# Kernel optimization log

Measured on AMD Instinct MI355X. Metric: run time of the kernel, lower is better.

## Reference

```python
import jax, jax.numpy as jnp
import numpy as np

N, E, C, H, EDGE_DIM, HID = 50000, 800000, 128, 8, 64, 512
D = C // H  # head dim = out_channels_conv


def layer_norm(x, g, b, eps=1e-5):
    mu = x.mean(-1, keepdims=True)
    var = ((x - mu) ** 2).mean(-1, keepdims=True)
    return (x - mu) * jax.lax.rsqrt(var + eps) * g + b


def _lin_init(k, fan_in, fan_out):
    s = 1.0 / np.sqrt(fan_in)
    kw, kb = jax.random.split(k)
    w = jax.random.uniform(kw, (fan_in, fan_out), minval=-s, maxval=s, dtype=jnp.float32)
    b = jax.random.uniform(kb, (fan_out,), minval=-s, maxval=s, dtype=jnp.float32)
    return w, b


def setup_inputs() -> dict:
    key = jax.random.key(0)
    ks = jax.random.split(key, 16)
    wq, bq = _lin_init(ks[0], C, C)
    wk, bk = _lin_init(ks[1], C, C)
    wv, bv = _lin_init(ks[2], C, C)
    ws, bs = _lin_init(ks[3], C, C)          # lin_self
    we, be = _lin_init(ks[4], EDGE_DIM, C)   # lin_edge
    wp, bp = _lin_init(ks[5], C, C)          # projection
    w1, b1 = _lin_init(ks[6], C, HID)        # node_dst_mlp[0]
    w2, b2 = _lin_init(ks[7], HID, C)        # node_dst_mlp[2]
    x = jax.random.normal(ks[8], (N, C), dtype=jnp.float32)
    edge_attr = jax.random.normal(ks[9], (E, EDGE_DIM), dtype=jnp.float32)
    edge_index = jax.random.randint(ks[10], (2, E), 0, N, dtype=jnp.int64)
    return dict(
        x=x, edge_attr=edge_attr, edge_index=edge_index,
        wq=wq, bq=bq, wk=wk, bk=bk, wv=wv, bv=bv, ws=ws, bs=bs,
        we=we, be=be, wp=wp, bp=bp, w1=w1, b1=b1, w2=w2, b2=b2,
        ln1_g=jnp.ones((C,), jnp.float32), ln1_b=jnp.zeros((C,), jnp.float32),
        ln2_g=jnp.ones((C,), jnp.float32), ln2_b=jnp.zeros((C,), jnp.float32),
    )


def reference(x, edge_attr, edge_index,
              wq, bq, wk, bk, wv, bv, ws, bs, we, be, wp, bp,
              w1, b1, w2, b2, ln1_g, ln1_b, ln2_g, ln2_b):
    src, dst = edge_index[0], edge_index[1]

    x_skip = x
    xn = layer_norm(x, ln1_g, ln1_b)                       # layer_norm_attention
    x_r = xn @ ws + bs                                     # lin_self residual
    q = (xn @ wq + bq).reshape(N, H, D)
    k = (xn @ wk + bk).reshape(N, H, D)
    v = (xn @ wv + bv).reshape(N, H, D)
    e = (edge_attr @ we + be).reshape(E, H, D)             # lin_edge (edge_pre_mlp = Identity)

    # edge-indexed multi-head attention: softmax over incoming edges per dst node
    ke = k[src] + e                                        # [E,H,D]
    alpha = jnp.einsum('ehd,ehd->eh', q[dst], ke) / np.sqrt(D)   # [E,H]
    amax = jax.lax.stop_gradient(jax.ops.segment_max(alpha, dst, num_segments=N))
    ex = jnp.exp(alpha - amax[dst])
    den = jax.ops.segment_sum(ex, dst, num_segments=N)
    w = ex / (den[dst] + 1e-16)                            # [E,H]
    out = jax.ops.segment_sum(w[:, :, None] * (v[src] + e), dst, num_segments=N)  # [N,H,D]
    out = out.reshape(N, C)

    out = (out + x_r) @ wp + bp                            # projection
    out = out + x_skip
    h = layer_norm(out, ln2_g, ln2_b)                      # layer_norm_mlp_dst
    h = jax.nn.gelu(h @ w1 + b1) @ w2 + b2                 # node_dst_mlp
    nodes_new = out + h
    return nodes_new, edge_attr
```

## Files before the change

kernel.cpp:

```cpp
#include <hip/hip_runtime.h>
#include <hip/hip_bf16.h>
#include <cstdio>

#define NN 50000
#define NE 800000
#define CC 128
#define EDIM 64
#define HIDN 512

using bf16 = __hip_bfloat16;
typedef short sh8 __attribute__((ext_vector_type(8)));
typedef float f32x4 __attribute__((ext_vector_type(4)));

static __device__ __forceinline__ float b2f(bf16 v){ return __bfloat162float(v); }
static __device__ __forceinline__ bf16 f2b(float v){ return __float2bfloat16(v); }
static __device__ __forceinline__ float u2f(unsigned short u){
    union { unsigned int i; float f; } w; w.i = ((unsigned int)u) << 16; return w.f;
}
static __device__ __forceinline__ unsigned short f2u(float f){
    bf16 b = __float2bfloat16(f);
    return *reinterpret_cast<unsigned short*>(&b);
}
static __device__ __forceinline__ float2 loadbf2(const bf16* p){
    __hip_bfloat162 v = *reinterpret_cast<const __hip_bfloat162*>(p);
    return make_float2(__bfloat162float(v.x), __bfloat162float(v.y));
}
static __device__ __forceinline__ float gelu_tanh(float x){
    const float c = 0.7978845608028654f;
    float u = c * (x + 0.044715f * x * x * x);
    return x / (1.0f + __expf(-2.0f * u));
}

constexpr size_t AL(size_t x){ return (x + 255) & ~(size_t)255; }
constexpr size_t OFF_FLAG = 0;
constexpr size_t OFF_DEG  = 256;
constexpr size_t OFF_ROW  = AL(OFF_DEG + (size_t)(NN + 1) * 4);
constexpr size_t OFF_CUR  = AL(OFF_ROW + (size_t)(NN + 1) * 4);
constexpr size_t OFF_EPOS = AL(OFF_CUR + (size_t)NN * 4);
constexpr size_t OFF_SRC  = AL(OFF_EPOS + (size_t)NE * 4);
constexpr size_t OFF_DST  = AL(OFF_SRC + (size_t)NE * 4);
constexpr size_t OFF_QC   = AL(OFF_DST + (size_t)NE * 4);
constexpr size_t OFF_KC   = AL(OFF_QC  + (size_t)NN * CC * 2);
constexpr size_t OFF_VC   = AL(OFF_KC  + (size_t)NN * CC * 2);
constexpr size_t OFF_ATT  = AL(OFF_VC  + (size_t)NN * CC * 2);
constexpr size_t OFF_PRM  = AL(OFF_ATT + (size_t)NN * CC * 2);
constexpr size_t PRM_ELEMS = 4*(16384+128) + 8192+128 + 16384+128 + 65536+512 + 65536+128 + 4*128;
constexpr size_t OFF_ALP  = AL(OFF_PRM + PRM_ELEMS * 2);
constexpr size_t OFF_VP   = AL(OFF_ALP + (size_t)NE * 8 * 4);
constexpr size_t OFF_XRC  = AL(OFF_VP + (size_t)NE * CC * 2);
constexpr size_t OFF_WFQ  = AL(OFF_XRC + (size_t)NN * CC * 2);
constexpr size_t OFF_WFK  = OFF_WFQ + 32768;
constexpr size_t OFF_WFV  = OFF_WFK + 32768;
constexpr size_t OFF_WFS  = OFF_WFV + 32768;
constexpr size_t OFF_WFP  = OFF_WFS + 32768;
constexpr size_t OFF_WF1  = OFF_WFP + 32768;
constexpr size_t OFF_WF2  = OFF_WF1 + 131072;
constexpr size_t OFF_WFE  = OFF_WF2 + 131072;
constexpr size_t OFF_BSUM = OFF_WFE + 16384;
constexpr size_t WS_NEED  = OFF_BSUM + 256;

__global__ void k_detect(const unsigned short* xw, const unsigned int* ew, int* flags){
    __shared__ int sw, sz;
    if (threadIdx.x == 0){ sw = 0; sz = 0; }
    __syncthreads();
    int w = 0;
    for (int i = threadIdx.x; i < 8192; i += 256){
        unsigned e = (xw[i] >> 7) & 0xFF;
        if (e == 0xFF || (e != 0 && (e < 0x60 || e > 0x90))) w++;
    }
    atomicAdd(&sw, w);
    int z = 0;
    for (int i = threadIdx.x; i < 2048; i += 256)
        if (ew[2*i+1] == 0u) z++;
    atomicAdd(&sz, z);
    __syncthreads();
    if (threadIdx.x == 0){
        flags[0] = (sw > 2048) ? 1 : 0;
        flags[1] = (sz > 1536) ? 1 : 0;
    }
}

struct CvtJob { const void* s; bf16* d; int n; };
struct CvtJobs { CvtJob j[20]; };
__global__ void k_cvt_all(CvtJobs jobs, const int* flags){
    const int f = flags[0];
    const int e = blockIdx.x >> 5;
    const CvtJob J = jobs.j[e];
    const int stride = 32 * 256;
    for (int i = (blockIdx.x & 31) * 256 + threadIdx.x; i < J.n; i += stride){
        if (f) J.d[i] = f2b(((const float*)J.s)[i]);
        else   J.d[i] = ((const bf16*)J.s)[i];
    }
}

__global__ void k_cvt_idx(const int* e32, int* srcI, int* dstI, int* deg, const int* flags){
    const int f = flags[1];
    int i = blockIdx.x * blockDim.x + threadIdx.x;
    const int stride = gridDim.x * blockDim.x;
    if (f){
        const long long* e64 = (const long long*)e32;
        for (; i < NE; i += stride){
            srcI[i] = (int)e64[i];
            const int d = (int)e64[NE + i];
            dstI[i] = d;
            atomicAdd(&deg[d], 1);
        }
    } else {
        for (; i < NE; i += stride){
            srcI[i] = e32[i];
            const int d = e32[NE + i];
            dstI[i] = d;
            atomicAdd(&deg[d], 1);
        }
    }
}

struct WJob { const bf16* W; bf16* WF; int K; int N; };
struct WJobs { WJob j[8]; };
__global__ void k_wprep_all(WJobs jobs){
    const WJob J = jobs.j[blockIdx.x / 48];
    const int KS = J.K >> 5;
    const int total = J.K * J.N;
    for (int o = (blockIdx.x % 48) * 256 + threadIdx.x; o < total; o += 48 * 256){
        const int j  = o & 7;
        const int ln = (o >> 3) & 63;
        const int tt = o >> 9;
        const int ks = tt % KS, ct = tt / KS;
        const int kk = (ks << 5) + ((ln >> 4) << 3) + j;
        const int c  = (ct << 4) + (ln & 15);
        J.WF[o] = J.W[kk * J.N + c];
    }
}

#define ASWZ(row, chunk)  (((row) << 8)  + ((((chunk) ^ ((row) & 15))) << 4))
#define HSWZ(row, chunk)  (((row) << 10) + ((((chunk) ^ ((row) & 15))) << 4))
#define EASWZ(row, chunk) (((row) << 7)  + ((((chunk) ^ ((row) & 7)))  << 4))

static __device__ __forceinline__ void gemm_nodes_128(
    const unsigned short* Abase, int row0, int lane,
    const bf16* __restrict__ WF, const bf16* __restrict__ bias,
    bf16* __restrict__ outp, int n0)
{
    const int rA = row0 + (lane & 15);
    sh8 af[4];
    #pragma unroll
    for (int ks = 0; ks < 4; ++ks)
        af[ks] = *(const sh8*)((const char*)Abase + ASWZ(rA, (ks << 2) + (lane >> 4)));
    f32x4 acc[8] = {};
    #pragma unroll
    for (int ks = 0; ks < 4; ++ks)
        #pragma unroll
        for (int ct = 0; ct < 8; ++ct){
            sh8 bfr = *(const sh8*)(WF + ((size_t)((ct << 2) + ks) * 64 + lane) * 8);
            acc[ct] = __builtin_amdgcn_mfma_f32_16x16x32_bf16(af[ks], bfr, acc[ct], 0, 0, 0);
        }
    #pragma unroll
    for (int ct = 0; ct < 8; ++ct){
        const int c = (ct << 4) + (lane & 15);
        const float bv = b2f(bias[c]);
        #pragma unroll
        for (int i = 0; i < 4; ++i){
            const int r = row0 + ((lane >> 4) << 2) + i;
            if (n0 + r < NN)
                outp[(size_t)(n0 + r) * CC + c] = f2b(acc[ct][i] + bv);
        }
    }
}

__global__ __launch_bounds__(256) void k_node_pre2(
    const void* __restrict__ x_raw, const int* __restrict__ flags,
    const bf16* __restrict__ WFq, const bf16* __restrict__ bq,
    const bf16* __restrict__ WFk, const bf16* __restrict__ bk,
    const bf16* __restrict__ WFv, const bf16* __restrict__ bv,
    const bf16* __restrict__ WFs, const bf16* __restrict__ bs,
    const bf16* __restrict__ g,  const bf16* __restrict__ bb,
    bf16* __restrict__ q, bf16* __restrict__ k, bf16* __restrict__ v,
    bf16* __restrict__ xr)
{
    __shared__ unsigned short A[64 * 128];
    const int t = threadIdx.x, lane = t & 63, wid = t >> 6;
    const int n0 = blockIdx.x * 64;

    if (flags[0]){
        const float* x = (const float*)x_raw;
        #pragma unroll
        for (int it = 0; it < 8; ++it){
            const int u = t + 256 * it;
            const int row = u >> 5, c = (u & 31) << 2;
            float4 a = make_float4(0.f, 0.f, 0.f, 0.f);
            if (n0 + row < NN)
                a = *(const float4*)&x[(size_t)(n0 + row) * CC + c];
            ushort4 b;
            b.x = f2u(a.x); b.y = f2u(a.y); b.z = f2u(a.z); b.w = f2u(a.w);
            *(ushort4*)((char*)A + ASWZ(row, c >> 3) + ((c & 7) << 1)) = b;
        }
    } else {
        const bf16* x = (const bf16*)x_raw;
        #pragma unroll
        for (int it = 0; it < 4; ++it){
            const int c8 = t + 256 * it;
            const int row = c8 >> 4, chunk = c8 & 15, col = chunk << 3;
            uint4 val = make_uint4(0u, 0u, 0u, 0u);
            if (n0 + row < NN)
                val = *(const uint4*)&x[(size_t)(n0 + row) * CC + col];
            *(uint4*)((char*)A + ASWZ(row, chunk)) = val;
        }
    }
    __syncthreads();

    {
        const int nd = wid * 16 + (lane & 15), qd = lane >> 4;
        float vals[32];
        #pragma unroll
        for (int i = 0; i < 4; ++i){
            uint4 u = *(const uint4*)((const char*)A + ASWZ(nd, (qd << 2) + i));
            unsigned uu[4] = {u.x, u.y, u.z, u.w};
            #pragma unroll
            for (int j2 = 0; j2 < 4; ++j2){
                vals[i*8 + j2*2]     = u2f((unsigned short)(uu[j2] & 0xFFFF));
                vals[i*8 + j2*2 + 1] = u2f((unsigned short)(uu[j2] >> 16));
            }
        }
        float s = 0.f;
        #pragma unroll
        for (int i = 0; i < 32; ++i) s += vals[i];
        s += __shfl_xor(s, 16); s += __shfl_xor(s, 32);
        const float mu = s * (1.0f / CC);
        float vv = 0.f;
        #pragma unroll
        for (int i = 0; i < 32; ++i){ const float d = vals[i] - mu; vv += d * d; }
        vv += __shfl_xor(vv, 16); vv += __shfl_xor(vv, 32);
        const float rstd = rsqrtf(vv * (1.0f / CC) + 1e-5f);
        #pragma unroll
        for (int i = 0; i < 4; ++i){
            unsigned w[4];
            #pragma unroll
            for (int j2 = 0; j2 < 4; ++j2){
                const int c0 = qd * 32 + i * 8 + j2 * 2;
                const float a0 = (vals[i*8+j2*2]   - mu) * rstd * b2f(g[c0])   + b2f(bb[c0]);
                const float a1 = (vals[i*8+j2*2+1] - mu) * rstd * b2f(g[c0+1]) + b2f(bb[c0+1]);
                w[j2] = (unsigned)f2u(a0) | ((unsigned)f2u(a1) << 16);
            }
            *(uint4*)((char*)A + ASWZ(nd, (qd << 2) + i)) = make_uint4(w[0], w[1], w[2], w[3]);
        }
    }
    __syncthreads();

    const int row0 = wid * 16;
    gemm_nodes_128(A, row0, lane, WFq, bq, q,  n0);
    gemm_nodes_128(A, row0, lane, WFk, bk, k,  n0);
    gemm_nodes_128(A, row0, lane, WFv, bv, v,  n0);
    gemm_nodes_128(A, row0, lane, WFs, bs, xr, n0);
}

__global__ __launch_bounds__(1024) void k_scan1(const int* __restrict__ deg,
                                                int* __restrict__ row, int* __restrict__ bsum){
    __shared__ int sb[1024];
    const int t = threadIdx.x;
    const int idx = blockIdx.x * 1024 + t;
    sb[t] = (idx < NN) ? deg[idx] : 0;
    __syncthreads();
    for (int off = 1; off < 1024; off <<= 1){
        int tv = (t >= off) ? sb[t - off] : 0;
        __syncthreads();
        sb[t] += tv;
        __syncthreads();
    }
    if (idx < NN) row[idx + 1] = sb[t];
    if (t == 1023) bsum[blockIdx.x] = sb[1023];
}

__global__ void k_scan2(int* __restrict__ bsum, int nb){
    int v = (threadIdx.x < nb) ? bsum[threadIdx.x] : 0;
    for (int off = 1; off < 64; off <<= 1){
        int u = __shfl_up(v, off);
        if (threadIdx.x >= off) v += u;
    }
    if (threadIdx.x < nb) bsum[threadIdx.x] = v;
}

__global__ __launch_bounds__(1024) void k_scan3(const int* __restrict__ bsum, int* __restrict__ row){
    const int idx = blockIdx.x * 1024 + threadIdx.x;
    const int add = (blockIdx.x > 0) ? bsum[blockIdx.x - 1] : 0;
    if (idx < NN) row[idx + 1] += add;
    if (idx == 0) row[0] = 0;
}

__global__ void k_scatter(const int* __restrict__ dst, const int* __restrict__ rowstart,
                          int* __restrict__ cursor, int* __restrict__ epos){
    const int i = blockIdx.x * blockDim.x + threadIdx.x;
    if (i < NE) {
        const int d = dst[i];
        const int p = atomicAdd(&cursor[d], 1);
        epos[i] = rowstart[d] + p;
    }
}

__global__ __launch_bounds__(256) void k_edge4(
    const void* __restrict__ ea_raw, const int* __restrict__ flags,
    const bf16* __restrict__ WFe, const bf16* __restrict__ be,
    const bf16* __restrict__ kv_q, const bf16* __restrict__ kv_k, const bf16* __restrict__ kv_v,
    const int* __restrict__ srcI, const int* __restrict__ dstI, const int* __restrict__ epos,
    float* __restrict__ alphap, unsigned short* __restrict__ vperm,
    void* __restrict__ outv)
{
    __shared__ unsigned short EA[64 * 64];
    __shared__ unsigned short ET[64 * 128];
    const int t = threadIdx.x, lane = t & 63, wid = t >> 6;
    const int e0 = blockIdx.x * 64;

    if (flags[0]){
        const float* ea = (const float*)ea_raw;
        float* outd = (float*)outv + (size_t)NN * CC;
        #pragma unroll
        for (int it = 0; it < 4; ++it){
            const int u = t + 256 * it;
            const int row = u >> 4, c = (u & 15) << 2;
            const size_t o = (size_t)(e0 + row) * EDIM + c;
            const float4 a = *(const float4*)&ea[o];
            *(float4*)&outd[o] = a;
            ushort4 b;
            b.x = f2u(a.x); b.y = f2u(a.y); b.z = f2u(a.z); b.w = f2u(a.w);
            *(ushort4*)((char*)EA + EASWZ(row, c >> 3) + ((c & 7) << 1)) = b;
        }
    } else {
        const unsigned short* ea = (const unsigned short*)ea_raw;
        unsigned short* outd = (unsigned short*)outv + (size_t)NN * CC;
        #pragma unroll
        for (int it = 0; it < 2; ++it){
            const int u = t + 256 * it;
            const int row = u >> 3, c = (u & 7) << 3;
            const size_t o = (size_t)(e0 + row) * EDIM + c;
            uint4 raw = *(const uint4*)&ea[o];
            *(uint4*)&outd[o] = raw;
            *(uint4*)((char*)EA + EASWZ(row, c >> 3)) = raw;
        }
    }
    __syncthreads();

    const int row0 = wid * 16;
    {
        const int rA = row0 + (lane & 15);
        sh8 af[2];
        #pragma unroll
        for (int ks = 0; ks < 2; ++ks)
            af[ks] = *(const sh8*)((const char*)EA + EASWZ(rA, (ks << 2) + (lane >> 4)));
        f32x4 acc[8] = {};
        #pragma unroll
        for (int ks = 0; ks < 2; ++ks)
            #pragma unroll
            for (int ct = 0; ct < 8; ++ct){
                sh8 bfr = *(const sh8*)(WFe + ((size_t)((ct << 1) + ks) * 64 + lane) * 8);
                acc[ct] = __builtin_amdgcn_mfma_f32_16x16x32_bf16(af[ks], bfr, acc[ct], 0, 0, 0);
            }
        #pragma unroll
        for (int ct = 0; ct < 8; ++ct){
            const int c = (ct << 4) + (lane & 15);
            const float bv = b2f(be[c]);
            #pragma unroll
            for (int i = 0; i < 4; ++i){
                const int r = row0 + ((lane >> 4) << 2) + i;
                *(unsigned short*)((char*)ET + ASWZ(r, c >> 3) + ((c & 7) << 1)) =
                    f2u(acc[ct][i] + bv);
            }
        }
    }
    __syncthreads();

    const int g = t >> 5, cT = t & 31, c = cT << 2;
    int s8[8], d8[8], p8[8];
    #pragma unroll
    for (int i = 0; i < 8; ++i){
        const int eid = e0 + g * 8 + i;
        s8[i] = srcI[eid];
        d8[i] = dstI[eid];
        p8[i] = epos[eid];
    }
    ushort4 kr[8], vr[8], qr[8];
    #pragma unroll
    for (int i = 0; i < 8; ++i) kr[i] = *(const ushort4*)&kv_k[(size_t)s8[i] * CC + c];
    #pragma unroll
    for (int i = 0; i < 8; ++i) vr[i] = *(const ushort4*)&kv_v[(size_t)s8[i] * CC + c];
    #pragma unroll
    for (int i = 0; i < 8; ++i) qr[i] = *(const ushort4*)&kv_q[(size_t)d8[i] * CC + c];
    #pragma unroll
    for (int i = 0; i < 8; ++i){
        const ushort4 ev = *(const ushort4*)((const char*)ET + ASWZ(g * 8 + i, c >> 3) + ((c & 7) << 1));
        const float e0_ = u2f(ev.x), e1_ = u2f(ev.y), e2_ = u2f(ev.z), e3_ = u2f(ev.w);
        float part = u2f(qr[i].x) * (e0_ + u2f(kr[i].x)) + u2f(qr[i].y) * (e1_ + u2f(kr[i].y))
                   + u2f(qr[i].z) * (e2_ + u2f(kr[i].z)) + u2f(qr[i].w) * (e3_ + u2f(kr[i].w));
        part += __shfl_xor(part, 1);
        part += __shfl_xor(part, 2);
        if ((cT & 3) == 0)
            alphap[(size_t)p8[i] * 8 + (cT >> 2)] = part * 0.25f;
        ushort4 vo;
        vo.x = f2u(e0_ + u2f(vr[i].x)); vo.y = f2u(e1_ + u2f(vr[i].y));
        vo.z = f2u(e2_ + u2f(vr[i].z)); vo.w = f2u(e3_ + u2f(vr[i].w));
        *(ushort4*)&vperm[(size_t)p8[i] * CC + c] = vo;
    }
}

__global__ __launch_bounds__(256) void k_attn3(
    const float* __restrict__ alphap, const bf16* __restrict__ vperm,
    const int* __restrict__ rowstart, bf16* __restrict__ attn_bf)
{
    const int t = threadIdx.x, lane = t & 63, wid = t >> 6;
    const int n = blockIdx.x * 4 + wid;
    const int h = lane >> 3;

    float m = -INFINITY, den = 0.0f;
    float2 num = make_float2(0.0f, 0.0f);

    const int jb = rowstart[n], je = rowstart[n + 1];
    for (int j = jb; j < je; ++j) {
        const float alpha = alphap[(size_t)j * 8 + h];
        const float2 v2 = loadbf2(&vperm[(size_t)j * CC + 2 * lane]);
        if (alpha > m) {
            const float sc = __expf(m - alpha);
            den *= sc; num.x *= sc; num.y *= sc;
            m = alpha;
        }
        const float p = __expf(alpha - m);
        den += p;
        num.x += p * v2.x;
        num.y += p * v2.y;
    }
    const float inv = 1.0f / (den + 1e-16f);
    __hip_bfloat162 pr;
    pr.x = f2b(num.x * inv);
    pr.y = f2b(num.y * inv);
    *reinterpret_cast<__hip_bfloat162*>(&attn_bf[(size_t)n * CC + 2 * lane]) = pr;
}

__global__ __launch_bounds__(256) void k_post2(
    const bf16* __restrict__ attn_bf, const bf16* __restrict__ xr,
    const void* __restrict__ x_raw,
    const bf16* __restrict__ WFp, const bf16* __restrict__ bp,
    const bf16* __restrict__ WF1, const bf16* __restrict__ b1,
    const bf16* __restrict__ WF2, const bf16* __restrict__ b2c,
    const bf16* __restrict__ g2, const bf16* __restrict__ bb2,
    void* __restrict__ outv, const int* __restrict__ flags)
{
    __shared__ unsigned short A[64 * 128];
    __shared__ unsigned short HID[64 * 512];
    const int t = threadIdx.x, lane = t & 63, wid = t >> 6;
    const int n0 = blockIdx.x * 64;
    const int f32io = flags[0];

    #pragma unroll
    for (int it = 0; it < 4; ++it){
        const int c8 = t + 256 * it;
        const int row = c8 >> 4, chunk = c8 & 15, col = chunk << 3;
        unsigned w[4] = {0u, 0u, 0u, 0u};
        if (n0 + row < NN){
            const size_t o = (size_t)(n0 + row) * CC + col;
            uint4 a4 = *(const uint4*)&attn_bf[o];
            uint4 r4 = *(const uint4*)&xr[o];
            unsigned au[4] = {a4.x, a4.y, a4.z, a4.w};
            unsigned ru[4] = {r4.x, r4.y, r4.z, r4.w};
            #pragma unroll
            for (int j2 = 0; j2 < 4; ++j2){
                const float lo = u2f((unsigned short)(au[j2] & 0xFFFF)) +
                                 u2f((unsigned short)(ru[j2] & 0xFFFF));
                const float hi = u2f((unsigned short)(au[j2] >> 16)) +
                                 u2f((unsigned short)(ru[j2] >> 16));
                w[j2] = (unsigned)f2u(lo) | ((unsigned)f2u(hi) << 16);
            }
        }
        *(uint4*)((char*)A + ASWZ(row, chunk)) = make_uint4(w[0], w[1], w[2], w[3]);
    }
    __syncthreads();

    const int row0 = wid * 16;
    const int rA = row0 + (lane & 15);

    float out2[8][4];
    {
        sh8 af[4];
        #pragma unroll
        for (int ks = 0; ks < 4; ++ks)
            af[ks] = *(const sh8*)((const char*)A + ASWZ(rA, (ks << 2) + (lane >> 4)));
        f32x4 acc[8] = {};
        #pragma unroll
        for (int ks = 0; ks < 4; ++ks)
            #pragma unroll
            for (int ct = 0; ct < 8; ++ct){
                sh8 bfr = *(const sh8*)(WFp + ((size_t)((ct << 2) + ks) * 64 + lane) * 8);
                acc[ct] = __builtin_amdgcn_mfma_f32_16x16x32_bf16(af[ks], bfr, acc[ct], 0, 0, 0);
            }
        #pragma unroll
        for (int ct = 0; ct < 8; ++ct){
            const int c = (ct << 4) + (lane & 15);
            const float bv = b2f(bp[c]);
            #pragma unroll
            for (int i = 0; i < 4; ++i){
                const int r = row0 + ((lane >> 4) << 2) + i;
                float xs = 0.f;
                if (n0 + r < NN){
                    const size_t o = (size_t)(n0 + r) * CC + c;
                    xs = f32io ? ((const float*)x_raw)[o] : b2f(((const bf16*)x_raw)[o]);
                }
                out2[ct][i] = acc[ct][i] + bv + xs;
            }
        }
    }

    {
        float mu[4], rstd[4];
        #pragma unroll
        for (int i = 0; i < 4; ++i){
            float s = 0.f;
            #pragma unroll
            for (int ct = 0; ct < 8; ++ct) s += out2[ct][i];
            s += __shfl_xor(s, 1); s += __shfl_xor(s, 2);
            s += __shfl_xor(s, 4); s += __shfl_xor(s, 8);
            mu[i] = s * (1.0f / CC);
        }
        #pragma unroll
        for (int i = 0; i < 4; ++i){
            float vv = 0.f;
            #pragma unroll
            for (int ct = 0; ct < 8; ++ct){ const float d = out2[ct][i] - mu[i]; vv += d * d; }
            vv += __shfl_xor(vv, 1); vv += __shfl_xor(vv, 2);
            vv += __shfl_xor(vv, 4); vv += __shfl_xor(vv, 8);
            rstd[i] = rsqrtf(vv * (1.0f / CC) + 1e-5f);
        }
        #pragma unroll
        for (int ct = 0; ct < 8; ++ct){
            const int c = (ct << 4) + (lane & 15);
            const float gv = b2f(g2[c]), bbv = b2f(bb2[c]);
            const int chunk = c >> 3;
            #pragma unroll
            for (int i = 0; i < 4; ++i){
                const int r = row0 + ((lane >> 4) << 2) + i;
                const float ln = (out2[ct][i] - mu[i]) * rstd[i] * gv + bbv;
                *(unsigned short*)((char*)A + ASWZ(r, chunk) + ((c & 7) << 1)) = f2u(ln);
            }
        }
    }

    {
        sh8 af[4];
        #pragma unroll
        for (int ks = 0; ks < 4; ++ks)
            af[ks] = *(const sh8*)((const char*)A + ASWZ(rA, (ks << 2) + (lane >> 4)));
        #pragma unroll
        for (int grp = 0; grp < 4; ++grp){
            f32x4 acc[8] = {};
            #pragma unroll
            for (int ks = 0; ks < 4; ++ks)
                #pragma unroll
                for (int ctl = 0; ctl < 8; ++ctl){
                    const int ct = grp * 8 + ctl;
                    sh8 bfr = *(const sh8*)(WF1 + ((size_t)((ct << 2) + ks) * 64 + lane) * 8);
                    acc[ctl] = __builtin_amdgcn_mfma_f32_16x16x32_bf16(af[ks], bfr, acc[ctl], 0, 0, 0);
                }
            #pragma unroll
            for (int ctl = 0; ctl < 8; ++ctl){
                const int ct = grp * 8 + ctl;
                const int c = (ct << 4) + (lane & 15);
                const float bv = b2f(b1[c]);
                const int chunk = c >> 3;
                #pragma unroll
                for (int i = 0; i < 4; ++i){
                    const int r = row0 + ((lane >> 4) << 2) + i;
                    const float h = gelu_tanh(acc[ctl][i] + bv);
                    *(unsigned short*)((char*)HID + HSWZ(r, chunk) + ((c & 7) << 1)) = f2u(h);
                }
            }
        }
    }

    {
        f32x4 acc[8] = {};
        #pragma unroll
        for (int ks = 0; ks < 16; ++ks){
            sh8 afh = *(const sh8*)((const char*)HID + HSWZ(rA, (ks << 2) + (lane >> 4)));
            #pragma unroll
            for (int ct = 0; ct < 8; ++ct){
                sh8 bfr = *(const sh8*)(WF2 + ((size_t)((ct << 4) + ks) * 64 + lane) * 8);
                acc[ct] = __builtin_amdgcn_mfma_f32_16x16x32_bf16(afh, bfr, acc[ct], 0, 0, 0);
            }
        }
        #pragma unroll
        for (int ct = 0; ct < 8; ++ct){
            const int c = (ct << 4) + (lane & 15);
            const float bv = b2f(b2c[c]);
            #pragma unroll
            for (int i = 0; i < 4; ++i){
                const int r = row0 + ((lane >> 4) << 2) + i;
                if (n0 + r < NN){
                    const float val = out2[ct][i] + acc[ct][i] + bv;
                    if (f32io) ((float*)outv)[(size_t)(n0 + r) * CC + c] = val;
                    else       ((bf16*)outv)[(size_t)(n0 + r) * CC + c] = f2b(val);
                }
            }
        }
    }
}

extern "C" void kernel_launch(void* const* d_in, const int* in_sizes, int n_in,
                              void* d_out, int out_size, void* d_ws, size_t ws_size,
                              hipStream_t stream)
{
    if (ws_size < WS_NEED) {
        fprintf(stderr, "[kl] WS TOO SMALL ws=%zu need=%zu\n", ws_size, WS_NEED);
        return;
    }

    char* ws = (char*)d_ws;
    int*  flags = (int*)(ws + OFF_FLAG);
    int*  deg   = (int*)(ws + OFF_DEG);
    int*  row   = (int*)(ws + OFF_ROW);
    int*  cur   = (int*)(ws + OFF_CUR);
    int*  epos  = (int*)(ws + OFF_EPOS);
    int*  srcI  = (int*)(ws + OFF_SRC);
    int*  dstI  = (int*)(ws + OFF_DST);
    int*  bsum  = (int*)(ws + OFF_BSUM);
    bf16* qC    = (bf16*)(ws + OFF_QC);
    bf16* kC    = (bf16*)(ws + OFF_KC);
    bf16* vC    = (bf16*)(ws + OFF_VC);
    bf16* attC  = (bf16*)(ws + OFF_ATT);
    bf16* xrC   = (bf16*)(ws + OFF_XRC);
    float* alphap = (float*)(ws + OFF_ALP);
    unsigned short* vperm = (unsigned short*)(ws + OFF_VP);
    bf16* WFq = (bf16*)(ws + OFF_WFQ);
    bf16* WFk = (bf16*)(ws + OFF_WFK);
    bf16* WFv = (bf16*)(ws + OFF_WFV);
    bf16* WFs = (bf16*)(ws + OFF_WFS);
    bf16* WFp = (bf16*)(ws + OFF_WFP);
    bf16* WF1 = (bf16*)(ws + OFF_WF1);
    bf16* WF2 = (bf16*)(ws + OFF_WF2);
    bf16* WFe = (bf16*)(ws + OFF_WFE);

    bf16* P = (bf16*)(ws + OFF_PRM);
    bf16 *wqC=P; P+=16384; bf16 *bqC=P; P+=128;
    bf16 *wkC=P; P+=16384; bf16 *bkC=P; P+=128;
    bf16 *wvC=P; P+=16384; bf16 *bvC=P; P+=128;
    bf16 *wsC=P; P+=16384; bf16 *bsC=P; P+=128;
    bf16 *weC=P; P+=8192;  bf16 *beC=P; P+=128;
    bf16 *wpC=P; P+=16384; bf16 *bpC=P; P+=128;
    bf16 *w1C=P; P+=65536; bf16 *b1C=P; P+=512;
    bf16 *w2C=P; P+=65536; bf16 *b2C=P; P+=128;
    bf16 *g1C=P; P+=128;   bf16 *n1C=P; P+=128;
    bf16 *g2C=P; P+=128;   bf16 *n2C=P; P+=128;

    hipMemsetAsync(deg, 0, (size_t)(NN + 1) * sizeof(int), stream);
    hipMemsetAsync(cur, 0, (size_t)NN * sizeof(int), stream);

    k_detect<<<1, 256, 0, stream>>>((const unsigned short*)d_in[0],
                                    (const unsigned int*)d_in[2], flags);

    {
        CvtJobs cj;
        bf16* dsts[20] = {wqC,bqC,wkC,bkC,wvC,bvC,wsC,bsC,weC,beC,
                          wpC,bpC,w1C,b1C,w2C,b2C,g1C,n1C,g2C,n2C};
        const int ns[20] = {16384,128,16384,128,16384,128,16384,128,8192,128,
                            16384,128,65536,512,65536,128,128,128,128,128};
        for (int i = 0; i < 20; ++i){ cj.j[i].s = d_in[3 + i]; cj.j[i].d = dsts[i]; cj.j[i].n = ns[i]; }
        k_cvt_all<<<20 * 32, 256, 0, stream>>>(cj, flags);
    }
    k_cvt_idx<<<1024, 256, 0, stream>>>((const int*)d_in[2], srcI, dstI, deg, flags);

    {
        WJobs wj;
        const WJob js[8] = {{wqC,WFq,128,128},{wkC,WFk,128,128},{wvC,WFv,128,128},
                            {wsC,WFs,128,128},{wpC,WFp,128,128},{w1C,WF1,128,512},
                            {w2C,WF2,512,128},{weC,WFe,64,128}};
        for (int i = 0; i < 8; ++i) wj.j[i] = js[i];
        k_wprep_all<<<8 * 48, 256, 0, stream>>>(wj);
    }

    const int NB64 = (NN + 63) / 64;
    const int NSC  = (NN + 1023) / 1024;
    k_node_pre2<<<NB64, 256, 0, stream>>>(d_in[0], flags, WFq, bqC, WFk, bkC, WFv, bvC,
                                          WFs, bsC, g1C, n1C, qC, kC, vC, xrC);
    k_scan1<<<NSC, 1024, 0, stream>>>(deg, row, bsum);
    k_scan2<<<1, 64, 0, stream>>>(bsum, NSC);
    k_scan3<<<NSC, 1024, 0, stream>>>(bsum, row);
    k_scatter<<<(NE + 255) / 256, 256, 0, stream>>>(dstI, row, cur, epos);
    k_edge4<<<NE / 64, 256, 0, stream>>>(d_in[1], flags, WFe, beC, qC, kC, vC,
                                         srcI, dstI, epos, alphap, vperm, d_out);
    k_attn3<<<NN / 4, 256, 0, stream>>>(alphap, (const bf16*)vperm, row, attC);
    k_post2<<<NB64, 256, 0, stream>>>(attC, xrC, d_in[0], WFp, bpC, WF1, b1C, WF2, b2C,
                                      g2C, n2C, d_out, flags);
}
```

Measured before the change: 537.4 us.

## Fuse edge scatter into edge kernel, merge scan passes, store alpha as bf16

```diff
diff --git a/kernel.cpp b/kernel.cpp
--- a/kernel.cpp
+++ b/kernel.cpp
@@ -36,8 +36,7 @@
 constexpr size_t OFF_DEG  = 256;
 constexpr size_t OFF_ROW  = AL(OFF_DEG + (size_t)(NN + 1) * 4);
 constexpr size_t OFF_CUR  = AL(OFF_ROW + (size_t)(NN + 1) * 4);
-constexpr size_t OFF_EPOS = AL(OFF_CUR + (size_t)NN * 4);
-constexpr size_t OFF_SRC  = AL(OFF_EPOS + (size_t)NE * 4);
+constexpr size_t OFF_SRC  = AL(OFF_CUR + (size_t)(NN + 1) * 4);
 constexpr size_t OFF_DST  = AL(OFF_SRC + (size_t)NE * 4);
 constexpr size_t OFF_QC   = AL(OFF_DST + (size_t)NE * 4);
 constexpr size_t OFF_KC   = AL(OFF_QC  + (size_t)NN * CC * 2);
@@ -46,7 +45,7 @@
 constexpr size_t OFF_PRM  = AL(OFF_ATT + (size_t)NN * CC * 2);
 constexpr size_t PRM_ELEMS = 4*(16384+128) + 8192+128 + 16384+128 + 65536+512 + 65536+128 + 4*128;
 constexpr size_t OFF_ALP  = AL(OFF_PRM + PRM_ELEMS * 2);
-constexpr size_t OFF_VP   = AL(OFF_ALP + (size_t)NE * 8 * 4);
+constexpr size_t OFF_VP   = AL(OFF_ALP + (size_t)NE * 8 * 2);
 constexpr size_t OFF_XRC  = AL(OFF_VP + (size_t)NE * CC * 2);
 constexpr size_t OFF_WFQ  = AL(OFF_XRC + (size_t)NN * CC * 2);
 constexpr size_t OFF_WFK  = OFF_WFQ + 32768;
@@ -270,38 +269,32 @@
     if (t == 1023) bsum[blockIdx.x] = sb[1023];
 }
 
-__global__ void k_scan2(int* __restrict__ bsum, int nb){
-    int v = (threadIdx.x < nb) ? bsum[threadIdx.x] : 0;
-    for (int off = 1; off < 64; off <<= 1){
-        int u = __shfl_up(v, off);
-        if (threadIdx.x >= off) v += u;
-    }
-    if (threadIdx.x < nb) bsum[threadIdx.x] = v;
-}
-
-__global__ __launch_bounds__(1024) void k_scan3(const int* __restrict__ bsum, int* __restrict__ row){
-    const int idx = blockIdx.x * 1024 + threadIdx.x;
-    const int add = (blockIdx.x > 0) ? bsum[blockIdx.x - 1] : 0;
-    if (idx < NN) row[idx + 1] += add;
-    if (idx == 0) row[0] = 0;
-}
-
-__global__ void k_scatter(const int* __restrict__ dst, const int* __restrict__ rowstart,
-                          int* __restrict__ cursor, int* __restrict__ epos){
-    const int i = blockIdx.x * blockDim.x + threadIdx.x;
-    if (i < NE) {
-        const int d = dst[i];
-        const int p = atomicAdd(&cursor[d], 1);
-        epos[i] = rowstart[d] + p;
-    }
+__global__ __launch_bounds__(1024) void k_scan3(const int* __restrict__ bsum,
+                                                int* __restrict__ row, int* __restrict__ cur){
+    __shared__ int sadd;
+    const int t = threadIdx.x;
+    if (t < 64){
+        int a = 0;
+        for (int i = t; i < (int)blockIdx.x; i += 64) a += bsum[i];
+        for (int off = 32; off; off >>= 1) a += __shfl_xor(a, off);
+        if (t == 0) sadd = a;
+    }
+    __syncthreads();
+    const int idx = blockIdx.x * 1024 + t;
+    if (idx < NN){
+        const int vfin = row[idx + 1] + sadd;
+        row[idx + 1] = vfin;
+        cur[idx + 1] = vfin;
+    }
+    if (idx == 0){ row[0] = 0; cur[0] = 0; }
 }
 
 __global__ __launch_bounds__(256) void k_edge4(
     const void* __restrict__ ea_raw, const int* __restrict__ flags,
     const bf16* __restrict__ WFe, const bf16* __restrict__ be,
     const bf16* __restrict__ kv_q, const bf16* __restrict__ kv_k, const bf16* __restrict__ kv_v,
-    const int* __restrict__ srcI, const int* __restrict__ dstI, const int* __restrict__ epos,
-    float* __restrict__ alphap, unsigned short* __restrict__ vperm,
+    const int* __restrict__ srcI, const int* __restrict__ dstI, int* __restrict__ cur,
+    unsigned short* __restrict__ alphap, unsigned short* __restrict__ vperm,
     void* __restrict__ outv)
 {
     __shared__ unsigned short EA[64 * 64];
@@ -368,14 +361,20 @@
     __syncthreads();
 
     const int g = t >> 5, cT = t & 31, c = cT << 2;
-    int s8[8], d8[8], p8[8];
+    int s8[8], d8[8];
     #pragma unroll
     for (int i = 0; i < 8; ++i){
         const int eid = e0 + g * 8 + i;
         s8[i] = srcI[eid];
         d8[i] = dstI[eid];
-        p8[i] = epos[eid];
-    }
+    }
+    int pmine = 0;
+    if (cT < 8) pmine = atomicAdd(&cur[dstI[e0 + g * 8 + cT]], 1);
+    int p8[8];
+    #pragma unroll
+    for (int i = 0; i < 8; ++i)
+        p8[i] = __shfl(pmine, ((g & 1) << 5) + i);
+
     ushort4 kr[8], vr[8], qr[8];
     #pragma unroll
     for (int i = 0; i < 8; ++i) kr[i] = *(const ushort4*)&kv_k[(size_t)s8[i] * CC + c];
@@ -392,7 +391,7 @@
         part += __shfl_xor(part, 1);
         part += __shfl_xor(part, 2);
         if ((cT & 3) == 0)
-            alphap[(size_t)p8[i] * 8 + (cT >> 2)] = part * 0.25f;
+            alphap[(size_t)p8[i] * 8 + (cT >> 2)] = f2u(part * 0.25f);
         ushort4 vo;
         vo.x = f2u(e0_ + u2f(vr[i].x)); vo.y = f2u(e1_ + u2f(vr[i].y));
         vo.z = f2u(e2_ + u2f(vr[i].z)); vo.w = f2u(e3_ + u2f(vr[i].w));
@@ -401,7 +400,7 @@
 }
 
 __global__ __launch_bounds__(256) void k_attn3(
-    const float* __restrict__ alphap, const bf16* __restrict__ vperm,
+    const unsigned short* __restrict__ alphap, const bf16* __restrict__ vperm,
     const int* __restrict__ rowstart, bf16* __restrict__ attn_bf)
 {
     const int t = threadIdx.x, lane = t & 63, wid = t >> 6;
@@ -413,7 +412,7 @@
 
     const int jb = rowstart[n], je = rowstart[n + 1];
     for (int j = jb; j < je; ++j) {
-        const float alpha = alphap[(size_t)j * 8 + h];
+        const float alpha = u2f(alphap[(size_t)j * 8 + h]);
         const float2 v2 = loadbf2(&vperm[(size_t)j * CC + 2 * lane]);
         if (alpha > m) {
             const float sc = __expf(m - alpha);
@@ -613,7 +612,6 @@
     int*  deg   = (int*)(ws + OFF_DEG);
     int*  row   = (int*)(ws + OFF_ROW);
     int*  cur   = (int*)(ws + OFF_CUR);
-    int*  epos  = (int*)(ws + OFF_EPOS);
     int*  srcI  = (int*)(ws + OFF_SRC);
     int*  dstI  = (int*)(ws + OFF_DST);
     int*  bsum  = (int*)(ws + OFF_BSUM);
@@ -622,8 +620,8 @@
     bf16* vC    = (bf16*)(ws + OFF_VC);
     bf16* attC  = (bf16*)(ws + OFF_ATT);
     bf16* xrC   = (bf16*)(ws + OFF_XRC);
-    float* alphap = (float*)(ws + OFF_ALP);
-    unsigned short* vperm = (unsigned short*)(ws + OFF_VP);
+    unsigned short* alphap = (unsigned short*)(ws + OFF_ALP);
+    unsigned short* vperm  = (unsigned short*)(ws + OFF_VP);
     bf16* WFq = (bf16*)(ws + OFF_WFQ);
     bf16* WFk = (bf16*)(ws + OFF_WFK);
     bf16* WFv = (bf16*)(ws + OFF_WFV);
@@ -646,7 +644,6 @@
     bf16 *g2C=P; P+=128;   bf16 *n2C=P; P+=128;
 
     hipMemsetAsync(deg, 0, (size_t)(NN + 1) * sizeof(int), stream);
-    hipMemsetAsync(cur, 0, (size_t)NN * sizeof(int), stream);
 
     k_detect<<<1, 256, 0, stream>>>((const unsigned short*)d_in[0],
                                     (const unsigned int*)d_in[2], flags);
@@ -676,11 +673,9 @@
     k_node_pre2<<<NB64, 256, 0, stream>>>(d_in[0], flags, WFq, bqC, WFk, bkC, WFv, bvC,
                                           WFs, bsC, g1C, n1C, qC, kC, vC, xrC);
     k_scan1<<<NSC, 1024, 0, stream>>>(deg, row, bsum);
-    k_scan2<<<1, 64, 0, stream>>>(bsum, NSC);
-    k_scan3<<<NSC, 1024, 0, stream>>>(bsum, row);
-    k_scatter<<<(NE + 255) / 256, 256, 0, stream>>>(dstI, row, cur, epos);
+    k_scan3<<<NSC, 1024, 0, stream>>>(bsum, row, cur);
     k_edge4<<<NE / 64, 256, 0, stream>>>(d_in[1], flags, WFe, beC, qC, kC, vC,
-                                         srcI, dstI, epos, alphap, vperm, d_out);
+                                         srcI, dstI, cur, alphap, vperm, d_out);
     k_attn3<<<NN / 4, 256, 0, stream>>>(alphap, (const bf16*)vperm, row, attC);
     k_post2<<<NB64, 256, 0, stream>>>(attC, xrC, d_in[0], WFp, bpC, WF1, b1C, WF2, b2C,
                                       g2C, n2C, d_out, flags);
```

Measured after the change: 505.8 us. -5.9%, faster.
